# Kernel tuning notes

Hardware: AMD Instinct MI355X
Metric: run time of the kernel (lower is better)

## Reference

```python
import jax, jax.numpy as jnp
import numpy as np

N_NODES = 50000
N_EDGES = 800000
HIDDEN = 128


def setup_inputs() -> dict:
    key = jax.random.key(0)
    k1, k2, k3, k4 = jax.random.split(key, 4)
    node_attr = jax.random.normal(k1, (N_NODES, HIDDEN), dtype=jnp.float32)
    edge_index = jax.random.randint(k2, (2, N_EDGES), 0, N_NODES, dtype=jnp.int64)
    # nn.Linear default init scale ~ 1/sqrt(fan_in)
    W = jax.random.normal(k3, (HIDDEN, HIDDEN), dtype=jnp.float32) / np.sqrt(HIDDEN)
    b = jax.random.normal(k4, (HIDDEN,), dtype=jnp.float32) / np.sqrt(HIDDEN)
    return {"node_attr": node_attr, "edge_index": edge_index, "W": W, "b": b}


def reference(node_attr, edge_index, W, b):
    n = node_attr.shape[0]
    # dense projection: h = x @ W^T + b  (torch nn.Linear convention)
    h = node_attr @ W.T + b  # [N, D]
    dst, src = edge_index[0], edge_index[1]
    # gather source-node features, scatter-sum into destination nodes
    agg = jax.ops.segment_sum(h[src], dst, num_segments=n)  # [N, D]
    # degree = in-degree of each destination node, +1 for self
    deg = jax.ops.segment_sum(jnp.ones_like(dst), dst, num_segments=n)  # [N]
    out = (h + agg) / (deg + 1).astype(h.dtype)[:, None]
    return out
```

## Files before the change

kernel.cpp:

```cpp
#include <hip/hip_runtime.h>

#define N_NODES 50000
#define N_EDGES 800000
#define HID 128
#define NP 391
#define NGRP 16
#define CAPG 256
#define PSTRIDE (NGRP * CAPG)
#define CAPC 2816
#define PC_PAD 32
#define SCAT_BLOCKS 512
#define EPB2 ((N_EDGES + SCAT_BLOCKS - 1) / SCAT_BLOCKS)
#define EPT 7
#define GEMM_BLOCKS ((N_NODES + 63) / 64)
#define NSL 4
#define SLICE4_U16 ((size_t)N_NODES * 32)

typedef float f4v __attribute__((ext_vector_type(4)));
typedef short s8v __attribute__((ext_vector_type(8)));
typedef unsigned short u16;

__device__ __forceinline__ u16 f2bf(float f) {
  union { float f; unsigned u; } v;
  v.f = f;
  const unsigned r = v.u + 0x7FFFu + ((v.u >> 16) & 1u);
  return (u16)(r >> 16);
}
__device__ __forceinline__ float bf2f(u16 h) {
  union { unsigned u; float f; } v;
  v.u = ((unsigned)h) << 16;
  return v.f;
}

__global__ __launch_bounds__(256) void init_k(const float* __restrict__ W,
                                              u16* __restrict__ Wb,
                                              int* __restrict__ pcnt) {
  const int b = blockIdx.x;
  if (b < 64) {
    const int i = b * 256 + threadIdx.x;
    Wb[i] = f2bf(W[i]);
  } else {
    const int i = (b - 64) * 256 + threadIdx.x;
    if (i < NP * NGRP * PC_PAD) pcnt[i] = 0;
  }
}

__global__ __launch_bounds__(256) void scat_k(const int* __restrict__ EI,
                                              int* __restrict__ pcnt,
                                              unsigned* __restrict__ part) {
  __shared__ int hist[NP], base[NP];
  const int b = blockIdx.x;
  const int t = threadIdx.x;
  const int g = b & (NGRP - 1);
  for (int i = t; i < NP; i += 256) hist[i] = 0;
  __syncthreads();
  const int e0 = b * EPB2;
  const int e1 = min(e0 + EPB2, N_EDGES);
  int dsts[EPT], srcs[EPT];
#pragma unroll
  for (int i = 0; i < EPT; ++i) {
    const int e = e0 + i * 256 + t;
    const bool ok = e < e1;
    dsts[i] = ok ? EI[e] : -1;
    srcs[i] = ok ? EI[N_EDGES + e] : 0;
  }
#pragma unroll
  for (int i = 0; i < EPT; ++i)
    if (dsts[i] >= 0) atomicAdd(&hist[dsts[i] >> 7], 1);
  __syncthreads();
  for (int i = t; i < NP; i += 256) {
    const int h = hist[i];
    int bs = 0;
    if (h > 0) bs = atomicAdd(pcnt + (i * NGRP + g) * PC_PAD, h);
    base[i] = i * PSTRIDE + g * CAPG + min(bs, CAPG);
    hist[i] = 0;
  }
  __syncthreads();
#pragma unroll
  for (int i = 0; i < EPT; ++i) {
    if (dsts[i] < 0) continue;
    const int p = dsts[i] >> 7;
    const int pos = atomicAdd(&hist[p], 1);
    const int gpos = base[p] + pos;
    if (gpos < p * PSTRIDE + (g + 1) * CAPG)
      part[gpos] = ((unsigned)srcs[i] << 7) | (unsigned)(dsts[i] & 127);
  }
}

__global__ __launch_bounds__(256) void p2g_k(const unsigned* __restrict__ part,
                                             const int* __restrict__ pcnt,
                                             int* __restrict__ colidx,
                                             int2* __restrict__ rp2,
                                             const float* __restrict__ X,
                                             const u16* __restrict__ Wb,
                                             const float* __restrict__ Bias,
                                             u16* __restrict__ Hb) {
  __shared__ int cnt[128], rs[129], cur[128];
  if (blockIdx.x < NP) {
    const int p = blockIdx.x;
    const int t = threadIdx.x;
    const int n0 = p * 128;
    const int nn = min(128, N_NODES - n0);
    const int pb = p * PSTRIDE;
    if (t < 128) cnt[t] = 0;
    __syncthreads();
    for (int g = 0; g < NGRP; ++g) {
      const int n = min(pcnt[(p * NGRP + g) * PC_PAD], CAPG);
      for (int i = t; i < n; i += 256) atomicAdd(&cnt[part[pb + g * CAPG + i] & 127u], 1);
    }
    __syncthreads();
    if (t == 0) {
      int acc = 0;
      for (int i = 0; i < 128; ++i) { rs[i] = acc; acc += cnt[i]; }
      rs[128] = acc;
    }
    __syncthreads();
    if (t < 128) cur[t] = rs[t];
    if (t < nn) rp2[n0 + t] = make_int2(p * CAPC + rs[t], cnt[t]);
    __syncthreads();
    for (int g = 0; g < NGRP; ++g) {
      const int n = min(pcnt[(p * NGRP + g) * PC_PAD], CAPG);
      for (int i = t; i < n; i += 256) {
        const unsigned v = part[pb + g * CAPG + i];
        const int pos = atomicAdd(&cur[v & 127u], 1);
        if (pos < CAPC) colidx[p * CAPC + pos] = (int)(v >> 7);
      }
    }
    return;
  }
  const int gb = blockIdx.x - NP;
  const int lane = threadIdx.x & 63;
  const int wv = threadIdx.x >> 6;
  const int i0 = gb * 64 + wv * 16;
  const int r16 = lane & 15;
  const int kb = lane >> 4;

  int arow = i0 + r16;
  if (arow >= N_NODES) arow = N_NODES - 1;

  s8v a[4];
#pragma unroll
  for (int kc = 0; kc < 4; ++kc) {
    const int k0 = kc * 32 + kb * 8;
    const float4 x0 = *(const float4*)(X + (size_t)arow * HID + k0);
    const float4 x1 = *(const float4*)(X + (size_t)arow * HID + k0 + 4);
    s8v tv;
    tv[0] = (short)f2bf(x0.x); tv[1] = (short)f2bf(x0.y);
    tv[2] = (short)f2bf(x0.z); tv[3] = (short)f2bf(x0.w);
    tv[4] = (short)f2bf(x1.x); tv[5] = (short)f2bf(x1.y);
    tv[6] = (short)f2bf(x1.z); tv[7] = (short)f2bf(x1.w);
    a[kc] = tv;
  }

  f4v acc[8];
#pragma unroll
  for (int jt = 0; jt < 8; ++jt) acc[jt] = (f4v){0.f, 0.f, 0.f, 0.f};

#pragma unroll
  for (int jt = 0; jt < 8; ++jt) {
    const int j = jt * 16 + r16;
#pragma unroll
    for (int kc = 0; kc < 4; ++kc) {
      const int k0 = kc * 32 + kb * 8;
      const s8v bb = *(const s8v*)(Wb + (size_t)j * HID + k0);
      acc[jt] = __builtin_amdgcn_mfma_f32_16x16x32_bf16(a[kc], bb, acc[jt], 0, 0, 0);
    }
  }

#pragma unroll
  for (int jt = 0; jt < 8; ++jt) {
    const int sl = jt >> 1;
    const int c = (jt & 1) * 16 + r16;
    const float bias = Bias[jt * 16 + r16];
#pragma unroll
    for (int r = 0; r < 4; ++r) {
      const int row = i0 + kb * 4 + r;
      if (row < N_NODES)
        Hb[(size_t)sl * SLICE4_U16 + (size_t)row * 32 + c] = f2bf(acc[jt][r] + bias);
    }
  }
}

__global__ __launch_bounds__(256) void gather4_k(const u16* __restrict__ Hb,
                                                 const int* __restrict__ colidx,
                                                 const int2* __restrict__ rp2,
                                                 float* __restrict__ OUT) {
  const int slice = blockIdx.x & 3;
  const int nb = blockIdx.x >> 2;
  const int wv = threadIdx.x >> 6;
  const int lane = threadIdx.x & 63;
  const int q = lane >> 2;
  const int sl4 = lane & 3;
  const int node = (nb * 4 + wv) * 16 + q;
  const bool valid = node < N_NODES;
  const int nd = valid ? node : 0;
  const int2 bd = rp2[nd];
  const int b0 = bd.x;
  const int deg = bd.y;
  const u16* Hbs = Hb + (size_t)slice * SLICE4_U16;
  const int c0 = sl4 * 8;

  int src[8];
#pragma unroll
  for (int r = 0; r < 8; ++r) {
    const int idx = r * 4 + sl4;
    src[r] = (idx < deg) ? colidx[b0 + idx] : 0;
  }

  const s8v selfv = *(const s8v*)(Hbs + (size_t)nd * 32 + c0);

  f4v acc0 = {0.f, 0.f, 0.f, 0.f};
  f4v acc1 = {0.f, 0.f, 0.f, 0.f};

#pragma unroll
  for (int j0 = 0; j0 < 32; j0 += 8) {
    if (!__any(j0 < deg)) break;
    s8v v[8];
    float msk[8];
#pragma unroll
    for (int jj = 0; jj < 8; ++jj) {
      const int j = j0 + jj;
      int s = __shfl(src[j >> 2], q * 4 + (j & 3), 64);
      if (j >= deg) s = 0;
      msk[jj] = (j < deg) ? 1.f : 0.f;
      v[jj] = *(const s8v*)(Hbs + (size_t)s * 32 + c0);
    }
#pragma unroll
    for (int jj = 0; jj < 8; ++jj) {
#pragma unroll
      for (int t = 0; t < 4; ++t) {
        acc0[t] += bf2f((u16)v[jj][t]) * msk[jj];
        acc1[t] += bf2f((u16)v[jj][t + 4]) * msk[jj];
      }
    }
  }

  for (int j0 = 32; __any(j0 < deg); j0 += 8) {
    s8v v[8];
    float msk[8];
#pragma unroll
    for (int jj = 0; jj < 8; ++jj) {
      const int idx = j0 + jj;
      int s = (idx < deg) ? colidx[b0 + idx] : 0;
      msk[jj] = (idx < deg) ? 1.f : 0.f;
      v[jj] = *(const s8v*)(Hbs + (size_t)s * 32 + c0);
    }
#pragma unroll
    for (int jj = 0; jj < 8; ++jj) {
#pragma unroll
      for (int t = 0; t < 4; ++t) {
        acc0[t] += bf2f((u16)v[jj][t]) * msk[jj];
        acc1[t] += bf2f((u16)v[jj][t + 4]) * msk[jj];
      }
    }
  }

  if (valid) {
    const float inv = 1.0f / (float)(deg + 1);
    f4v o0, o1;
#pragma unroll
    for (int t = 0; t < 4; ++t) {
      o0[t] = (acc0[t] + bf2f((u16)selfv[t])) * inv;
      o1[t] = (acc1[t] + bf2f((u16)selfv[t + 4])) * inv;
    }
    float* po = OUT + (size_t)node * HID + slice * 32 + sl4 * 8;
    *(f4v*)(po) = o0;
    *(f4v*)(po + 4) = o1;
  }
}

extern "C" void kernel_launch(void* const* d_in, const int* in_sizes, int n_in,
                              void* d_out, int out_size, void* d_ws, size_t ws_size,
                              hipStream_t stream) {
  const float* X = (const float*)d_in[0];
  const int* EI = (const int*)d_in[1];
  const float* W = (const float*)d_in[2];
  const float* Bias = (const float*)d_in[3];

  float* OUT = (float*)d_out;

  char* ws = (char*)d_ws;
  u16* Hb = (u16*)(ws);
  unsigned* part = (unsigned*)(ws + 12800000);
  int* colidx = (int*)(ws + 19206144);
  int2* rp2 = (int2*)(ws + 23610368);
  int* pcnt = (int*)(ws + 24010368);
  u16* Wb = (u16*)(ws + 24811136);

  init_k<<<64 + (NP * NGRP * PC_PAD + 255) / 256, 256, 0, stream>>>(W, Wb, pcnt);
  scat_k<<<SCAT_BLOCKS, 256, 0, stream>>>(EI, pcnt, part);
  p2g_k<<<NP + GEMM_BLOCKS, 256, 0, stream>>>(part, pcnt, colidx, rp2, X, Wb, Bias, Hb);
  gather4_k<<<NSL * ((N_NODES + 63) / 64), 256, 0, stream>>>(Hb, colidx, rp2, OUT);
}
```

Before: 81.43 us.

## Co-schedule GEMM with edge scatter and split CSR build into own kernel

Moves the bf16 MFMA projection blocks from the partition-to-CSR kernel into the edge-scatter kernel, so the GEMM runs concurrently with the scatter instead of with the CSR build. The CSR build becomes a standalone kernel whose loop flattens the per-group iteration into one strided pass over all group slots, using a shared table of group counts. This aims to hide scatter atomics and latency behind GEMM work and to shorten the CSR pass. The trade-off is that the CSR kernel now runs alone with only 391 blocks, and the flattened loop visits empty slots.

```diff
diff --git a/kernel.cpp b/kernel.cpp
--- a/kernel.cpp
+++ b/kernel.cpp
@@ -45,90 +45,54 @@
   }
 }
 
-__global__ __launch_bounds__(256) void scat_k(const int* __restrict__ EI,
-                                              int* __restrict__ pcnt,
-                                              unsigned* __restrict__ part) {
-  __shared__ int hist[NP], base[NP];
-  const int b = blockIdx.x;
-  const int t = threadIdx.x;
-  const int g = b & (NGRP - 1);
-  for (int i = t; i < NP; i += 256) hist[i] = 0;
-  __syncthreads();
-  const int e0 = b * EPB2;
-  const int e1 = min(e0 + EPB2, N_EDGES);
-  int dsts[EPT], srcs[EPT];
-#pragma unroll
-  for (int i = 0; i < EPT; ++i) {
-    const int e = e0 + i * 256 + t;
-    const bool ok = e < e1;
-    dsts[i] = ok ? EI[e] : -1;
-    srcs[i] = ok ? EI[N_EDGES + e] : 0;
-  }
-#pragma unroll
-  for (int i = 0; i < EPT; ++i)
-    if (dsts[i] >= 0) atomicAdd(&hist[dsts[i] >> 7], 1);
-  __syncthreads();
-  for (int i = t; i < NP; i += 256) {
-    const int h = hist[i];
-    int bs = 0;
-    if (h > 0) bs = atomicAdd(pcnt + (i * NGRP + g) * PC_PAD, h);
-    base[i] = i * PSTRIDE + g * CAPG + min(bs, CAPG);
-    hist[i] = 0;
-  }
-  __syncthreads();
-#pragma unroll
-  for (int i = 0; i < EPT; ++i) {
-    if (dsts[i] < 0) continue;
-    const int p = dsts[i] >> 7;
-    const int pos = atomicAdd(&hist[p], 1);
-    const int gpos = base[p] + pos;
-    if (gpos < p * PSTRIDE + (g + 1) * CAPG)
-      part[gpos] = ((unsigned)srcs[i] << 7) | (unsigned)(dsts[i] & 127);
-  }
-}
-
-__global__ __launch_bounds__(256) void p2g_k(const unsigned* __restrict__ part,
-                                             const int* __restrict__ pcnt,
-                                             int* __restrict__ colidx,
-                                             int2* __restrict__ rp2,
+__global__ __launch_bounds__(256) void sg2_k(const int* __restrict__ EI,
+                                             int* __restrict__ pcnt,
+                                             unsigned* __restrict__ part,
                                              const float* __restrict__ X,
                                              const u16* __restrict__ Wb,
                                              const float* __restrict__ Bias,
                                              u16* __restrict__ Hb) {
-  __shared__ int cnt[128], rs[129], cur[128];
-  if (blockIdx.x < NP) {
-    const int p = blockIdx.x;
+  __shared__ int hist[NP], base[NP];
+  if (blockIdx.x < SCAT_BLOCKS) {
+    const int b = blockIdx.x;
     const int t = threadIdx.x;
-    const int n0 = p * 128;
-    const int nn = min(128, N_NODES - n0);
-    const int pb = p * PSTRIDE;
-    if (t < 128) cnt[t] = 0;
+    const int g = b & (NGRP - 1);
+    for (int i = t; i < NP; i += 256) hist[i] = 0;
     __syncthreads();
-    for (int g = 0; g < NGRP; ++g) {
-      const int n = min(pcnt[(p * NGRP + g) * PC_PAD], CAPG);
-      for (int i = t; i < n; i += 256) atomicAdd(&cnt[part[pb + g * CAPG + i] & 127u], 1);
-    }
+    const int e0 = b * EPB2;
+    const int e1 = min(e0 + EPB2, N_EDGES);
+    int dsts[EPT], srcs[EPT];
+#pragma unroll
+    for (int i = 0; i < EPT; ++i) {
+      const int e = e0 + i * 256 + t;
+      const bool ok = e < e1;
+      dsts[i] = ok ? EI[e] : -1;
+      srcs[i] = ok ? EI[N_EDGES + e] : 0;
+    }
+#pragma unroll
+    for (int i = 0; i < EPT; ++i)
+      if (dsts[i] >= 0) atomicAdd(&hist[dsts[i] >> 7], 1);
     __syncthreads();
-    if (t == 0) {
-      int acc = 0;
-      for (int i = 0; i < 128; ++i) { rs[i] = acc; acc += cnt[i]; }
-      rs[128] = acc;
+    for (int i = t; i < NP; i += 256) {
+      const int h = hist[i];
+      int bs = 0;
+      if (h > 0) bs = atomicAdd(pcnt + (i * NGRP + g) * PC_PAD, h);
+      base[i] = i * PSTRIDE + g * CAPG + min(bs, CAPG);
+      hist[i] = 0;
     }
     __syncthreads();
-    if (t < 128) cur[t] = rs[t];
-    if (t < nn) rp2[n0 + t] = make_int2(p * CAPC + rs[t], cnt[t]);
-    __syncthreads();
-    for (int g = 0; g < NGRP; ++g) {
-      const int n = min(pcnt[(p * NGRP + g) * PC_PAD], CAPG);
-      for (int i = t; i < n; i += 256) {
-        const unsigned v = part[pb + g * CAPG + i];
-        const int pos = atomicAdd(&cur[v & 127u], 1);
-        if (pos < CAPC) colidx[p * CAPC + pos] = (int)(v >> 7);
-      }
+#pragma unroll
+    for (int i = 0; i < EPT; ++i) {
+      if (dsts[i] < 0) continue;
+      const int p = dsts[i] >> 7;
+      const int pos = atomicAdd(&hist[p], 1);
+      const int gpos = base[p] + pos;
+      if (gpos < p * PSTRIDE + (g + 1) * CAPG)
+        part[gpos] = ((unsigned)srcs[i] << 7) | (unsigned)(dsts[i] & 127);
     }
     return;
   }
-  const int gb = blockIdx.x - NP;
+  const int gb = blockIdx.x - SCAT_BLOCKS;
   const int lane = threadIdx.x & 63;
   const int wv = threadIdx.x >> 6;
   const int i0 = gb * 64 + wv * 16;
@@ -177,6 +141,42 @@
       const int row = i0 + kb * 4 + r;
       if (row < N_NODES)
         Hb[(size_t)sl * SLICE4_U16 + (size_t)row * 32 + c] = f2bf(acc[jt][r] + bias);
+    }
+  }
+}
+
+__global__ __launch_bounds__(256) void p2csr_k(const unsigned* __restrict__ part,
+                                               const int* __restrict__ pcnt,
+                                               int* __restrict__ colidx,
+                                               int2* __restrict__ rp2) {
+  __shared__ int gcnt[NGRP], cnt[128], rs[129], cur[128];
+  const int p = blockIdx.x;
+  const int t = threadIdx.x;
+  const int n0 = p * 128;
+  const int nn = min(128, N_NODES - n0);
+  const int pb = p * PSTRIDE;
+  if (t < NGRP) gcnt[t] = min(pcnt[(p * NGRP + t) * PC_PAD], CAPG);
+  if (t < 128) cnt[t] = 0;
+  __syncthreads();
+  for (int idx = t; idx < PSTRIDE; idx += 256) {
+    if ((idx & (CAPG - 1)) < gcnt[idx >> 8])
+      atomicAdd(&cnt[part[pb + idx] & 127u], 1);
+  }
+  __syncthreads();
+  if (t == 0) {
+    int acc = 0;
+    for (int i = 0; i < 128; ++i) { rs[i] = acc; acc += cnt[i]; }
+    rs[128] = acc;
+  }
+  __syncthreads();
+  if (t < 128) cur[t] = rs[t];
+  if (t < nn) rp2[n0 + t] = make_int2(p * CAPC + rs[t], cnt[t]);
+  __syncthreads();
+  for (int idx = t; idx < PSTRIDE; idx += 256) {
+    if ((idx & (CAPG - 1)) < gcnt[idx >> 8]) {
+      const unsigned v = part[pb + idx];
+      const int pos = atomicAdd(&cur[v & 127u], 1);
+      if (pos < CAPC) colidx[p * CAPC + pos] = (int)(v >> 7);
     }
   }
 }
@@ -288,7 +288,7 @@
   u16* Wb = (u16*)(ws + 24811136);
 
   init_k<<<64 + (NP * NGRP * PC_PAD + 255) / 256, 256, 0, stream>>>(W, Wb, pcnt);
-  scat_k<<<SCAT_BLOCKS, 256, 0, stream>>>(EI, pcnt, part);
-  p2g_k<<<NP + GEMM_BLOCKS, 256, 0, stream>>>(part, pcnt, colidx, rp2, X, Wb, Bias, Hb);
+  sg2_k<<<SCAT_BLOCKS + GEMM_BLOCKS, 256, 0, stream>>>(EI, pcnt, part, X, Wb, Bias, Hb);
+  p2csr_k<<<NP, 256, 0, stream>>>(part, pcnt, colidx, rp2);
   gather4_k<<<NSL * ((N_NODES + 63) / 64), 256, 0, stream>>>(Hb, colidx, rp2, OUT);
 }
```

Measured after the change: 83.23 us. +2.2%, slower.
